# Kernel tuning notes

Hardware: AMD Instinct MI355X
Metric: run time of the kernel (lower is better)

Reference implementation:

```python
import jax, jax.numpy as jnp
import numpy as np

N = 10000
E = 320000
IN_DIM = 1
HD = 32
OUT_DIM = 1


def _lin(k, fan_in, fan_out):
    k1, k2 = jax.random.split(k)
    bound = 1.0 / np.sqrt(fan_in)
    W = jax.random.uniform(k1, (fan_in, fan_out), minval=-bound, maxval=bound, dtype=jnp.float32)
    b = jax.random.uniform(k2, (fan_out,), minval=-bound, maxval=bound, dtype=jnp.float32)
    return W, b


def setup_inputs() -> dict:
    key = jax.random.key(0)
    ks = jax.random.split(key, 12)
    sources = jax.random.randint(ks[0], (E,), 0, N)
    dests = jax.random.randint(ks[1], (E,), 0, N)
    weights = jax.random.uniform(ks[2], (E, 1), dtype=jnp.float32)
    x = jax.random.normal(ks[3], (N, IN_DIM), dtype=jnp.float32)
    h = jax.random.normal(ks[4], (N, HD), dtype=jnp.float32)
    W_enc, b_enc = _lin(ks[5], IN_DIM + HD, HD)
    W_msg, b_msg = _lin(ks[6], 2 * HD + 1, HD)
    W_upd, b_upd = _lin(ks[7], 2 * HD, HD)
    W_dec, b_dec = _lin(ks[8], 2 * HD, OUT_DIM)
    W_term, b_term = _lin(ks[9], HD, 1)
    W_pred, b_pred = _lin(ks[10], 2 * HD + 1, 1)
    return {"sources": sources, "dests": dests, "weights": weights, "x": x, "h": h,
            "W_enc": W_enc, "b_enc": b_enc, "W_msg": W_msg, "b_msg": b_msg,
            "W_upd": W_upd, "b_upd": b_upd, "W_dec": W_dec, "b_dec": b_dec,
            "W_term": W_term, "b_term": b_term, "W_pred": W_pred, "b_pred": b_pred}


def reference(sources, dests, weights, x, h, W_enc, b_enc, W_msg, b_msg,
              W_upd, b_upd, W_dec, b_dec, W_term, b_term, W_pred, b_pred):
    n = h.shape[0]
    # Encoder: z = Linear(cat[x, h])
    z = jnp.concatenate([x, h], axis=1) @ W_enc + b_enc  # [N, HD]
    # Processor messages: Linear(cat[z[dest], z[src], w])
    msg_in = jnp.concatenate([z[dests], z[sources], weights], axis=1)  # [E, 2*HD+1]
    messages = msg_in @ W_msg + b_msg  # [E, HD]
    # scatter-amax into destination nodes, -inf (no edge) -> 0
    m = jnp.full((n, HD), -jnp.inf, dtype=z.dtype).at[dests].max(messages)
    m = jnp.where(jnp.isneginf(m), jnp.zeros_like(m), m)
    h_new = jnp.concatenate([z, m], axis=1) @ W_upd + b_upd  # [N, HD]
    # Decoder
    y = jnp.concatenate([z, h_new], axis=1) @ W_dec + b_dec  # [N, 1]
    # Termination: proj of mean node state -> scalar
    t = (h_new.mean(axis=0) @ W_term + b_term).squeeze()
    # Predecessor: dense N x N score matrix, edge entries set to proj score
    pred_in = jnp.concatenate([h_new[dests], h_new[sources], weights], axis=1)
    edge_scores = (pred_in @ W_pred + b_pred)[:, 0]  # [E]
    p = jnp.full((n, n), -1e9, dtype=h_new.dtype).at[dests, sources].set(edge_scores)
    return (y, p, h_new, t)
```

## Files before the change

### kernel.cpp

```cpp
#include <hip/hip_runtime.h>
#include <stdint.h>

namespace {
constexpr int  kN  = 10000;
constexpr int  kE  = 320000;
constexpr long kPOff = 10000;
constexpr long kHOff = 10000L + 100000000L;
constexpr long kTOff = kHOff + 320000L;
}

typedef float f32x4 __attribute__((ext_vector_type(4)));

__device__ __forceinline__ float shfl32(float v, int k) { return __shfl(v, k, 32); }

__global__ __launch_bounds__(256) void encz_kernel(
    const float* __restrict__ x, const float* __restrict__ h,
    const float* __restrict__ W_enc, const float* __restrict__ b_enc,
    const float* __restrict__ W_msg, const float* __restrict__ b_msg,
    float* __restrict__ z, float* __restrict__ zwd, float* __restrict__ zws,
    float* __restrict__ m)
{
    int lane = threadIdx.x & 63;
    int wid  = threadIdx.x >> 6;
    int half = lane >> 5;
    int j    = lane & 31;
    int i = blockIdx.x * 8 + wid * 2 + half;
    if (i >= kN) return;

    float hj = h[(long)i * 32 + j];
    float xi = x[i];
    float zj = fmaf(xi, W_enc[j], b_enc[j]);
#pragma unroll
    for (int k = 0; k < 32; ++k)
        zj = fmaf(shfl32(hj, k), W_enc[(1 + k) * 32 + j], zj);

    z[(long)i * 32 + j] = zj;
    m[(long)i * 32 + j] = -__builtin_inff();

    float dv = b_msg[j], sv = 0.0f;
#pragma unroll
    for (int k = 0; k < 32; ++k) {
        float zk = shfl32(zj, k);
        dv = fmaf(zk, W_msg[k * 32 + j], dv);
        sv = fmaf(zk, W_msg[(32 + k) * 32 + j], sv);
    }
    zwd[(long)i * 32 + j] = dv;
    zws[(long)i * 32 + j] = sv;
}

__global__ __launch_bounds__(256) void msgmax_kernel(
    const int* __restrict__ src, const int* __restrict__ dst,
    const float* __restrict__ w, const float* __restrict__ zwd,
    const float* __restrict__ zws, const float* __restrict__ W_msg,
    float* __restrict__ m)
{
    int lane = threadIdx.x & 63;
    int wid  = threadIdx.x >> 6;
    int half = lane >> 5;
    int j    = lane & 31;
    float Ww = W_msg[64 * 32 + j];
    int gw = blockIdx.x * 4 + wid;
    int nw = gridDim.x * 4;
    for (int ep = gw; ep < kE / 2; ep += nw) {
        int e = ep * 2 + half;
        int d = dst[e], s = src[e];
        float val = fmaf(w[e], Ww, zwd[(long)d * 32 + j] + zws[(long)s * 32 + j]);
        float* addr = m + (long)d * 32 + j;
        if (val >= 0.0f)
            atomicMax(reinterpret_cast<int*>(addr), __float_as_int(val));
        else
            atomicMin(reinterpret_cast<unsigned int*>(addr), __float_as_uint(val));
    }
}

__global__ __launch_bounds__(256) void updn_kernel(
    const float* __restrict__ z, const float* __restrict__ m,
    const float* __restrict__ W_upd, const float* __restrict__ b_upd,
    const float* __restrict__ W_dec, const float* __restrict__ b_dec,
    const float* __restrict__ W_pred,
    float* __restrict__ y_out, float* __restrict__ h_out,
    float* __restrict__ a_out, float* __restrict__ b_out,
    float* __restrict__ partials)
{
    int i = blockIdx.x * 256 + threadIdx.x;
    bool valid = i < kN;
    int ii = valid ? i : (kN - 1);

    float acc[32];
#pragma unroll
    for (int jj = 0; jj < 32; ++jj) acc[jj] = b_upd[jj];
    float yv = b_dec[0];

    const float4* z4 = reinterpret_cast<const float4*>(z + (long)ii * 32);
#pragma unroll
    for (int q = 0; q < 8; ++q) {
        float4 v = z4[q];
        float in0 = v.x, in1 = v.y, in2 = v.z, in3 = v.w;
        int k = q * 4;
        yv = fmaf(in0, W_dec[k + 0], yv);
        yv = fmaf(in1, W_dec[k + 1], yv);
        yv = fmaf(in2, W_dec[k + 2], yv);
        yv = fmaf(in3, W_dec[k + 3], yv);
        const float* W0 = W_upd + (k + 0) * 32;
        const float* W1 = W_upd + (k + 1) * 32;
        const float* W2 = W_upd + (k + 2) * 32;
        const float* W3 = W_upd + (k + 3) * 32;
#pragma unroll
        for (int jj = 0; jj < 32; ++jj) acc[jj] = fmaf(in0, W0[jj], acc[jj]);
#pragma unroll
        for (int jj = 0; jj < 32; ++jj) acc[jj] = fmaf(in1, W1[jj], acc[jj]);
#pragma unroll
        for (int jj = 0; jj < 32; ++jj) acc[jj] = fmaf(in2, W2[jj], acc[jj]);
#pragma unroll
        for (int jj = 0; jj < 32; ++jj) acc[jj] = fmaf(in3, W3[jj], acc[jj]);
    }

    const float NEG_INF = -__builtin_inff();
    const float4* m4 = reinterpret_cast<const float4*>(m + (long)ii * 32);
#pragma unroll
    for (int q = 0; q < 8; ++q) {
        float4 v = m4[q];
        float in0 = (v.x == NEG_INF) ? 0.0f : v.x;
        float in1 = (v.y == NEG_INF) ? 0.0f : v.y;
        float in2 = (v.z == NEG_INF) ? 0.0f : v.z;
        float in3 = (v.w == NEG_INF) ? 0.0f : v.w;
        int k = 32 + q * 4;
        const float* W0 = W_upd + (k + 0) * 32;
        const float* W1 = W_upd + (k + 1) * 32;
        const float* W2 = W_upd + (k + 2) * 32;
        const float* W3 = W_upd + (k + 3) * 32;
#pragma unroll
        for (int jj = 0; jj < 32; ++jj) acc[jj] = fmaf(in0, W0[jj], acc[jj]);
#pragma unroll
        for (int jj = 0; jj < 32; ++jj) acc[jj] = fmaf(in1, W1[jj], acc[jj]);
#pragma unroll
        for (int jj = 0; jj < 32; ++jj) acc[jj] = fmaf(in2, W2[jj], acc[jj]);
#pragma unroll
        for (int jj = 0; jj < 32; ++jj) acc[jj] = fmaf(in3, W3[jj], acc[jj]);
    }

    float av = 0.0f, bv = 0.0f;
#pragma unroll
    for (int k = 0; k < 32; ++k) {
        yv = fmaf(acc[k], W_dec[32 + k], yv);
        av = fmaf(acc[k], W_pred[k], av);
        bv = fmaf(acc[k], W_pred[32 + k], bv);
    }

    if (valid) {
        y_out[i] = yv;
        a_out[i] = av;
        b_out[i] = bv;
        float4* hrow = reinterpret_cast<float4*>(h_out + (long)i * 32);
#pragma unroll
        for (int q = 0; q < 8; ++q)
            hrow[q] = make_float4(acc[q * 4 + 0], acc[q * 4 + 1], acc[q * 4 + 2], acc[q * 4 + 3]);
    }

    int wslot = blockIdx.x * 4 + ((threadIdx.x >> 6) & 3);
#pragma unroll
    for (int jj = 0; jj < 32; ++jj) {
        float v = valid ? acc[jj] : 0.0f;
#pragma unroll
        for (int off = 32; off; off >>= 1) v += __shfl_down(v, off, 64);
        if ((threadIdx.x & 63) == 0) partials[(long)wslot * 32 + jj] = v;
    }
}

__global__ void term_kernel(const float* __restrict__ partials,
                            const float* __restrict__ W_term,
                            const float* __restrict__ b_term,
                            float* __restrict__ t_out)
{
    int l = threadIdx.x;
    float s = 0.0f;
    if (l < 32) {
        for (int r = 0; r < 160; ++r) s += partials[(long)r * 32 + l];
        s = (s * (1.0f / (float)kN)) * W_term[l];
    }
#pragma unroll
    for (int off = 32; off; off >>= 1) s += __shfl_down(s, off, 64);
    if (l == 0) t_out[0] = s + b_term[0];
}

__global__ __launch_bounds__(256) void fill_kernel(float* __restrict__ p)
{
    long idx = (long)blockIdx.x * 256 + threadIdx.x;
    long stride = (long)gridDim.x * 256;
    const long total4 = (long)kN * (long)kN / 4;
    f32x4 v = { -1e9f, -1e9f, -1e9f, -1e9f };
    f32x4* p4 = reinterpret_cast<f32x4*>(p);
    for (long i = idx; i < total4; i += stride)
        p4[i] = v;
}

__global__ __launch_bounds__(256) void predl_kernel(
    const int* __restrict__ src, const int* __restrict__ dst,
    const float* __restrict__ w, const float* __restrict__ a,
    const float* __restrict__ b, const float* __restrict__ W_pred,
    const float* __restrict__ b_pred, float* __restrict__ p)
{
    int e = blockIdx.x * 256 + threadIdx.x;
    if (e >= kE) return;
    int d = dst[e], s = src[e];
    float score = a[d] + b[s] + fmaf(w[e], W_pred[64], b_pred[0]);
    p[(long)d * kN + s] = score;
}

extern "C" void kernel_launch(void* const* d_in, const int* in_sizes, int n_in,
                              void* d_out, int out_size, void* d_ws, size_t ws_size,
                              hipStream_t stream)
{
    const int*   sources = (const int*)d_in[0];
    const int*   dests   = (const int*)d_in[1];
    const float* weights = (const float*)d_in[2];
    const float* x       = (const float*)d_in[3];
    const float* h       = (const float*)d_in[4];
    const float* W_enc   = (const float*)d_in[5];
    const float* b_enc   = (const float*)d_in[6];
    const float* W_msg   = (const float*)d_in[7];
    const float* b_msg   = (const float*)d_in[8];
    const float* W_upd   = (const float*)d_in[9];
    const float* b_upd   = (const float*)d_in[10];
    const float* W_dec   = (const float*)d_in[11];
    const float* b_dec   = (const float*)d_in[12];
    const float* W_term  = (const float*)d_in[13];
    const float* b_term  = (const float*)d_in[14];
    const float* W_pred  = (const float*)d_in[15];
    const float* b_pred  = (const float*)d_in[16];

    float* out   = (float*)d_out;
    float* y_out = out;
    float* p_out = out + kPOff;
    float* h_out = out + kHOff;
    float* t_out = out + kTOff;

    float* z        = (float*)d_ws;
    float* m        = z   + (long)kN * 32;
    float* zwd      = m   + (long)kN * 32;
    float* zws      = zwd + (long)kN * 32;
    float* a_ws     = zws + (long)kN * 32;
    float* b_ws     = a_ws + kN;
    float* partials = b_ws + kN;

    encz_kernel<<<(kN + 7) / 8, 256, 0, stream>>>(x, h, W_enc, b_enc, W_msg, b_msg,
                                                  z, zwd, zws, m);
    msgmax_kernel<<<10000, 256, 0, stream>>>(sources, dests, weights, zwd, zws, W_msg, m);
    updn_kernel<<<(kN + 255) / 256, 256, 0, stream>>>(z, m, W_upd, b_upd, W_dec, b_dec,
                                                      W_pred, y_out, h_out, a_ws, b_ws,
                                                      partials);
    term_kernel<<<1, 64, 0, stream>>>(partials, W_term, b_term, t_out);
    fill_kernel<<<8192, 256, 0, stream>>>(p_out);
    predl_kernel<<<(kE + 255) / 256, 256, 0, stream>>>(sources, dests, weights, a_ws, b_ws,
                                                       W_pred, b_pred, p_out);
}
```

Baseline: 557.4 us.

## Replace atomic scatter-max with CSR build and per-node gather-max

Builds a destination-sorted edge list (degree histogram, single-block scan, atomic scatter into an edge list stored temporarily in the p output buffer), then computes each node's max message with a per-node gather loop instead of per-element float atomics. This removes atomic contention on the m buffer and the -inf init/fixup, and writes m directly with the zero fallback. It adds four extra kernel launches, a serial single-block scan, and a data-dependent loop whose length follows node degree. It also relies on fill_kernel later overwriting the reused p buffer.

After: 586.7 us. 5.3% more time.

```diff
diff --git a/kernel.cpp b/kernel.cpp
--- a/kernel.cpp
+++ b/kernel.cpp
@@ -18,8 +18,11 @@
     const float* __restrict__ W_enc, const float* __restrict__ b_enc,
     const float* __restrict__ W_msg, const float* __restrict__ b_msg,
     float* __restrict__ z, float* __restrict__ zwd, float* __restrict__ zws,
-    float* __restrict__ m)
-{
+    int* __restrict__ deg, int* __restrict__ cursor)
+{
+    int t = blockIdx.x * 256 + threadIdx.x;
+    if (t < kN) { deg[t] = 0; cursor[t] = 0; }
+
     int lane = threadIdx.x & 63;
     int wid  = threadIdx.x >> 6;
     int half = lane >> 5;
@@ -35,7 +38,6 @@
         zj = fmaf(shfl32(hj, k), W_enc[(1 + k) * 32 + j], zj);
 
     z[(long)i * 32 + j] = zj;
-    m[(long)i * 32 + j] = -__builtin_inff();
 
     float dv = b_msg[j], sv = 0.0f;
 #pragma unroll
@@ -48,29 +50,90 @@
     zws[(long)i * 32 + j] = sv;
 }
 
-__global__ __launch_bounds__(256) void msgmax_kernel(
-    const int* __restrict__ src, const int* __restrict__ dst,
-    const float* __restrict__ w, const float* __restrict__ zwd,
-    const float* __restrict__ zws, const float* __restrict__ W_msg,
+__global__ __launch_bounds__(256) void hist_kernel(const int* __restrict__ dst,
+                                                   int* __restrict__ deg)
+{
+    int e = blockIdx.x * 256 + threadIdx.x;
+    if (e < kE) atomicAdd(&deg[dst[e]], 1);
+}
+
+__global__ __launch_bounds__(256) void scan_kernel(const int* __restrict__ deg,
+                                                   int* __restrict__ rowptr)
+{
+    __shared__ int part[256];
+    const int CH = 40;
+    int t = threadIdx.x;
+    int vals[CH];
+    int local = 0;
+#pragma unroll
+    for (int i = 0; i < CH; ++i) {
+        int idx = t * CH + i;
+        int v = (idx < kN) ? deg[idx] : 0;
+        vals[i] = local;
+        local += v;
+    }
+    part[t] = local;
+    __syncthreads();
+    for (int off = 1; off < 256; off <<= 1) {
+        int v = (t >= off) ? part[t - off] : 0;
+        __syncthreads();
+        part[t] += v;
+        __syncthreads();
+    }
+    int excl = part[t] - local;
+#pragma unroll
+    for (int i = 0; i < CH; ++i) {
+        int idx = t * CH + i;
+        if (idx < kN) rowptr[idx] = excl + vals[i];
+    }
+}
+
+__global__ __launch_bounds__(256) void scatter_kernel(
+    const int* __restrict__ dst, const int* __restrict__ rowptr,
+    int* __restrict__ cursor, int* __restrict__ elist)
+{
+    int e = blockIdx.x * 256 + threadIdx.x;
+    if (e >= kE) return;
+    int d = dst[e];
+    int pos = atomicAdd(&cursor[d], 1);
+    elist[rowptr[d] + pos] = e;
+}
+
+__global__ __launch_bounds__(256) void gathermax_kernel(
+    const int* __restrict__ src, const float* __restrict__ w,
+    const float* __restrict__ zwd, const float* __restrict__ zws,
+    const int* __restrict__ rowptr, const int* __restrict__ deg,
+    const int* __restrict__ elist, const float* __restrict__ W_msg,
     float* __restrict__ m)
 {
     int lane = threadIdx.x & 63;
     int wid  = threadIdx.x >> 6;
     int half = lane >> 5;
     int j    = lane & 31;
+    int d = blockIdx.x * 8 + wid * 2 + half;
+    if (d >= kN) return;
+
     float Ww = W_msg[64 * 32 + j];
-    int gw = blockIdx.x * 4 + wid;
-    int nw = gridDim.x * 4;
-    for (int ep = gw; ep < kE / 2; ep += nw) {
-        int e = ep * 2 + half;
-        int d = dst[e], s = src[e];
-        float val = fmaf(w[e], Ww, zwd[(long)d * 32 + j] + zws[(long)s * 32 + j]);
-        float* addr = m + (long)d * 32 + j;
-        if (val >= 0.0f)
-            atomicMax(reinterpret_cast<int*>(addr), __float_as_int(val));
-        else
-            atomicMin(reinterpret_cast<unsigned int*>(addr), __float_as_uint(val));
-    }
+    float partial = zwd[(long)d * 32 + j];
+    float mx = -__builtin_inff();
+    int base = rowptr[d], cnt = deg[d];
+
+    if (cnt > 0) {
+        int e = elist[base];
+        int s = src[e];
+        float we = w[e];
+        for (int i = 1; i < cnt; ++i) {
+            int e2 = elist[base + i];
+            int s2 = src[e2];
+            float we2 = w[e2];
+            float msg = fmaf(we, Ww, partial + zws[(long)s * 32 + j]);
+            mx = fmaxf(mx, msg);
+            s = s2; we = we2;
+        }
+        float msg = fmaf(we, Ww, partial + zws[(long)s * 32 + j]);
+        mx = fmaxf(mx, msg);
+    }
+    m[(long)d * 32 + j] = (mx == -__builtin_inff()) ? 0.0f : mx;
 }
 
 __global__ __launch_bounds__(256) void updn_kernel(
@@ -242,10 +305,18 @@
     float* a_ws     = zws + (long)kN * 32;
     float* b_ws     = a_ws + kN;
     float* partials = b_ws + kN;
+    int*   deg      = (int*)(partials + 160 * 32);
+    int*   rowptr   = deg + kN;
+    int*   cursor   = rowptr + kN;
+    int*   elist    = (int*)p_out;
 
     encz_kernel<<<(kN + 7) / 8, 256, 0, stream>>>(x, h, W_enc, b_enc, W_msg, b_msg,
-                                                  z, zwd, zws, m);
-    msgmax_kernel<<<10000, 256, 0, stream>>>(sources, dests, weights, zwd, zws, W_msg, m);
+                                                  z, zwd, zws, deg, cursor);
+    hist_kernel<<<(kE + 255) / 256, 256, 0, stream>>>(dests, deg);
+    scan_kernel<<<1, 256, 0, stream>>>(deg, rowptr);
+    scatter_kernel<<<(kE + 255) / 256, 256, 0, stream>>>(dests, rowptr, cursor, elist);
+    gathermax_kernel<<<(kN + 7) / 8, 256, 0, stream>>>(sources, weights, zwd, zws,
+                                                       rowptr, deg, elist, W_msg, m);
     updn_kernel<<<(kN + 255) / 256, 256, 0, stream>>>(z, m, W_upd, b_upd, W_dec, b_dec,
                                                       W_pred, y_out, h_out, a_ws, b_ws,
                                                       partials);
```

## Spread dense score-matrix fill across compute kernels and merge termination into pred

Applied to the files above, without the earlier changes.

The 400MB fill of the -1e9 score matrix is split into three slices, each appended to the encoder, message-max and update kernels, so the bandwidth-bound fill runs alongside the latency-bound gather and atomic work. All kernels use a fixed grid of 2048 blocks with grid-stride loops. The separate term kernel is removed by accumulating the node-state sum with atomicAdd and computing t inside the pred kernel. This adds atomic float additions, which make the summation order nondeterministic, and fixes the fill split ratios by hand.

After: 599.1 us. 1.07x slower.

```diff
diff --git a/kernel.cpp b/kernel.cpp
--- a/kernel.cpp
+++ b/kernel.cpp
@@ -7,52 +7,70 @@
 constexpr long kPOff = 10000;
 constexpr long kHOff = 10000L + 100000000L;
 constexpr long kTOff = kHOff + 320000L;
+constexpr long kP4   = (long)kN * kN / 4;
+constexpr long kFillA = kP4 * 15 / 100;
+constexpr long kFillB = kP4 * 80 / 100;
+constexpr int  kG = 2048;
 }
 
 typedef float f32x4 __attribute__((ext_vector_type(4)));
 
 __device__ __forceinline__ float shfl32(float v, int k) { return __shfl(v, k, 32); }
 
-__global__ __launch_bounds__(256) void encz_kernel(
+__device__ __forceinline__ void fill_slice(float* __restrict__ p, long lo, long hi)
+{
+    long idx = (long)blockIdx.x * blockDim.x + threadIdx.x;
+    long stride = (long)gridDim.x * blockDim.x;
+    f32x4 v = { -1e9f, -1e9f, -1e9f, -1e9f };
+    f32x4* p4 = reinterpret_cast<f32x4*>(p);
+    for (long i = lo + idx; i < hi; i += stride)
+        p4[i] = v;
+}
+
+__global__ __launch_bounds__(256) void k1_encz(
     const float* __restrict__ x, const float* __restrict__ h,
     const float* __restrict__ W_enc, const float* __restrict__ b_enc,
     const float* __restrict__ W_msg, const float* __restrict__ b_msg,
     float* __restrict__ z, float* __restrict__ zwd, float* __restrict__ zws,
-    float* __restrict__ m)
-{
+    float* __restrict__ m, float* __restrict__ sum_h, float* __restrict__ p)
+{
+    if (blockIdx.x == 0 && threadIdx.x < 32) sum_h[threadIdx.x] = 0.0f;
+
     int lane = threadIdx.x & 63;
     int wid  = threadIdx.x >> 6;
     int half = lane >> 5;
     int j    = lane & 31;
-    int i = blockIdx.x * 8 + wid * 2 + half;
-    if (i >= kN) return;
-
-    float hj = h[(long)i * 32 + j];
-    float xi = x[i];
-    float zj = fmaf(xi, W_enc[j], b_enc[j]);
-#pragma unroll
-    for (int k = 0; k < 32; ++k)
-        zj = fmaf(shfl32(hj, k), W_enc[(1 + k) * 32 + j], zj);
-
-    z[(long)i * 32 + j] = zj;
-    m[(long)i * 32 + j] = -__builtin_inff();
-
-    float dv = b_msg[j], sv = 0.0f;
-#pragma unroll
-    for (int k = 0; k < 32; ++k) {
-        float zk = shfl32(zj, k);
-        dv = fmaf(zk, W_msg[k * 32 + j], dv);
-        sv = fmaf(zk, W_msg[(32 + k) * 32 + j], sv);
-    }
-    zwd[(long)i * 32 + j] = dv;
-    zws[(long)i * 32 + j] = sv;
-}
-
-__global__ __launch_bounds__(256) void msgmax_kernel(
+
+    for (int i = blockIdx.x * 8 + wid * 2 + half; i < kN; i += kG * 8) {
+        float hj = h[(long)i * 32 + j];
+        float xi = x[i];
+        float zj = fmaf(xi, W_enc[j], b_enc[j]);
+#pragma unroll
+        for (int k = 0; k < 32; ++k)
+            zj = fmaf(shfl32(hj, k), W_enc[(1 + k) * 32 + j], zj);
+
+        z[(long)i * 32 + j] = zj;
+        m[(long)i * 32 + j] = -__builtin_inff();
+
+        float dv = b_msg[j], sv = 0.0f;
+#pragma unroll
+        for (int k = 0; k < 32; ++k) {
+            float zk = shfl32(zj, k);
+            dv = fmaf(zk, W_msg[k * 32 + j], dv);
+            sv = fmaf(zk, W_msg[(32 + k) * 32 + j], sv);
+        }
+        zwd[(long)i * 32 + j] = dv;
+        zws[(long)i * 32 + j] = sv;
+    }
+
+    fill_slice(p, 0, kFillA);
+}
+
+__global__ __launch_bounds__(256) void k2_msgmax(
     const int* __restrict__ src, const int* __restrict__ dst,
     const float* __restrict__ w, const float* __restrict__ zwd,
     const float* __restrict__ zws, const float* __restrict__ W_msg,
-    float* __restrict__ m)
+    float* __restrict__ m, float* __restrict__ p)
 {
     int lane = threadIdx.x & 63;
     int wid  = threadIdx.x >> 6;
@@ -60,8 +78,7 @@
     int j    = lane & 31;
     float Ww = W_msg[64 * 32 + j];
     int gw = blockIdx.x * 4 + wid;
-    int nw = gridDim.x * 4;
-    for (int ep = gw; ep < kE / 2; ep += nw) {
+    for (int ep = gw; ep < kE / 2; ep += kG * 4) {
         int e = ep * 2 + half;
         int d = dst[e], s = src[e];
         float val = fmaf(w[e], Ww, zwd[(long)d * 32 + j] + zws[(long)s * 32 + j]);
@@ -71,140 +88,129 @@
         else
             atomicMin(reinterpret_cast<unsigned int*>(addr), __float_as_uint(val));
     }
-}
-
-__global__ __launch_bounds__(256) void updn_kernel(
+
+    fill_slice(p, kFillA, kFillB);
+}
+
+__global__ __launch_bounds__(256) void k3_updn(
     const float* __restrict__ z, const float* __restrict__ m,
     const float* __restrict__ W_upd, const float* __restrict__ b_upd,
     const float* __restrict__ W_dec, const float* __restrict__ b_dec,
     const float* __restrict__ W_pred,
     float* __restrict__ y_out, float* __restrict__ h_out,
     float* __restrict__ a_out, float* __restrict__ b_out,
-    float* __restrict__ partials)
+    float* __restrict__ sum_h, float* __restrict__ p)
 {
     int i = blockIdx.x * 256 + threadIdx.x;
-    bool valid = i < kN;
-    int ii = valid ? i : (kN - 1);
-
-    float acc[32];
-#pragma unroll
-    for (int jj = 0; jj < 32; ++jj) acc[jj] = b_upd[jj];
-    float yv = b_dec[0];
-
-    const float4* z4 = reinterpret_cast<const float4*>(z + (long)ii * 32);
-#pragma unroll
-    for (int q = 0; q < 8; ++q) {
-        float4 v = z4[q];
-        float in0 = v.x, in1 = v.y, in2 = v.z, in3 = v.w;
-        int k = q * 4;
-        yv = fmaf(in0, W_dec[k + 0], yv);
-        yv = fmaf(in1, W_dec[k + 1], yv);
-        yv = fmaf(in2, W_dec[k + 2], yv);
-        yv = fmaf(in3, W_dec[k + 3], yv);
-        const float* W0 = W_upd + (k + 0) * 32;
-        const float* W1 = W_upd + (k + 1) * 32;
-        const float* W2 = W_upd + (k + 2) * 32;
-        const float* W3 = W_upd + (k + 3) * 32;
-#pragma unroll
-        for (int jj = 0; jj < 32; ++jj) acc[jj] = fmaf(in0, W0[jj], acc[jj]);
-#pragma unroll
-        for (int jj = 0; jj < 32; ++jj) acc[jj] = fmaf(in1, W1[jj], acc[jj]);
-#pragma unroll
-        for (int jj = 0; jj < 32; ++jj) acc[jj] = fmaf(in2, W2[jj], acc[jj]);
-#pragma unroll
-        for (int jj = 0; jj < 32; ++jj) acc[jj] = fmaf(in3, W3[jj], acc[jj]);
-    }
-
-    const float NEG_INF = -__builtin_inff();
-    const float4* m4 = reinterpret_cast<const float4*>(m + (long)ii * 32);
-#pragma unroll
-    for (int q = 0; q < 8; ++q) {
-        float4 v = m4[q];
-        float in0 = (v.x == NEG_INF) ? 0.0f : v.x;
-        float in1 = (v.y == NEG_INF) ? 0.0f : v.y;
-        float in2 = (v.z == NEG_INF) ? 0.0f : v.z;
-        float in3 = (v.w == NEG_INF) ? 0.0f : v.w;
-        int k = 32 + q * 4;
-        const float* W0 = W_upd + (k + 0) * 32;
-        const float* W1 = W_upd + (k + 1) * 32;
-        const float* W2 = W_upd + (k + 2) * 32;
-        const float* W3 = W_upd + (k + 3) * 32;
-#pragma unroll
-        for (int jj = 0; jj < 32; ++jj) acc[jj] = fmaf(in0, W0[jj], acc[jj]);
-#pragma unroll
-        for (int jj = 0; jj < 32; ++jj) acc[jj] = fmaf(in1, W1[jj], acc[jj]);
-#pragma unroll
-        for (int jj = 0; jj < 32; ++jj) acc[jj] = fmaf(in2, W2[jj], acc[jj]);
-#pragma unroll
-        for (int jj = 0; jj < 32; ++jj) acc[jj] = fmaf(in3, W3[jj], acc[jj]);
-    }
-
-    float av = 0.0f, bv = 0.0f;
-#pragma unroll
-    for (int k = 0; k < 32; ++k) {
-        yv = fmaf(acc[k], W_dec[32 + k], yv);
-        av = fmaf(acc[k], W_pred[k], av);
-        bv = fmaf(acc[k], W_pred[32 + k], bv);
-    }
-
-    if (valid) {
-        y_out[i] = yv;
-        a_out[i] = av;
-        b_out[i] = bv;
-        float4* hrow = reinterpret_cast<float4*>(h_out + (long)i * 32);
-#pragma unroll
-        for (int q = 0; q < 8; ++q)
-            hrow[q] = make_float4(acc[q * 4 + 0], acc[q * 4 + 1], acc[q * 4 + 2], acc[q * 4 + 3]);
-    }
-
-    int wslot = blockIdx.x * 4 + ((threadIdx.x >> 6) & 3);
-#pragma unroll
-    for (int jj = 0; jj < 32; ++jj) {
-        float v = valid ? acc[jj] : 0.0f;
-#pragma unroll
-        for (int off = 32; off; off >>= 1) v += __shfl_down(v, off, 64);
-        if ((threadIdx.x & 63) == 0) partials[(long)wslot * 32 + jj] = v;
-    }
-}
-
-__global__ void term_kernel(const float* __restrict__ partials,
-                            const float* __restrict__ W_term,
-                            const float* __restrict__ b_term,
-                            float* __restrict__ t_out)
-{
-    int l = threadIdx.x;
-    float s = 0.0f;
-    if (l < 32) {
-        for (int r = 0; r < 160; ++r) s += partials[(long)r * 32 + l];
-        s = (s * (1.0f / (float)kN)) * W_term[l];
-    }
-#pragma unroll
-    for (int off = 32; off; off >>= 1) s += __shfl_down(s, off, 64);
-    if (l == 0) t_out[0] = s + b_term[0];
-}
-
-__global__ __launch_bounds__(256) void fill_kernel(float* __restrict__ p)
-{
-    long idx = (long)blockIdx.x * 256 + threadIdx.x;
-    long stride = (long)gridDim.x * 256;
-    const long total4 = (long)kN * (long)kN / 4;
-    f32x4 v = { -1e9f, -1e9f, -1e9f, -1e9f };
-    f32x4* p4 = reinterpret_cast<f32x4*>(p);
-    for (long i = idx; i < total4; i += stride)
-        p4[i] = v;
-}
-
-__global__ __launch_bounds__(256) void predl_kernel(
+    if (i < ((kN + 255) & ~255)) {
+        bool valid = i < kN;
+        int ii = valid ? i : (kN - 1);
+
+        float acc[32];
+#pragma unroll
+        for (int jj = 0; jj < 32; ++jj) acc[jj] = b_upd[jj];
+        float yv = b_dec[0];
+
+        const float4* z4 = reinterpret_cast<const float4*>(z + (long)ii * 32);
+#pragma unroll
+        for (int q = 0; q < 8; ++q) {
+            float4 v = z4[q];
+            float in0 = v.x, in1 = v.y, in2 = v.z, in3 = v.w;
+            int k = q * 4;
+            yv = fmaf(in0, W_dec[k + 0], yv);
+            yv = fmaf(in1, W_dec[k + 1], yv);
+            yv = fmaf(in2, W_dec[k + 2], yv);
+            yv = fmaf(in3, W_dec[k + 3], yv);
+            const float* W0 = W_upd + (k + 0) * 32;
+            const float* W1 = W_upd + (k + 1) * 32;
+            const float* W2 = W_upd + (k + 2) * 32;
+            const float* W3 = W_upd + (k + 3) * 32;
+#pragma unroll
+            for (int jj = 0; jj < 32; ++jj) acc[jj] = fmaf(in0, W0[jj], acc[jj]);
+#pragma unroll
+            for (int jj = 0; jj < 32; ++jj) acc[jj] = fmaf(in1, W1[jj], acc[jj]);
+#pragma unroll
+            for (int jj = 0; jj < 32; ++jj) acc[jj] = fmaf(in2, W2[jj], acc[jj]);
+#pragma unroll
+            for (int jj = 0; jj < 32; ++jj) acc[jj] = fmaf(in3, W3[jj], acc[jj]);
+        }
+
+        const float NEG_INF = -__builtin_inff();
+        const float4* m4 = reinterpret_cast<const float4*>(m + (long)ii * 32);
+#pragma unroll
+        for (int q = 0; q < 8; ++q) {
+            float4 v = m4[q];
+            float in0 = (v.x == NEG_INF) ? 0.0f : v.x;
+            float in1 = (v.y == NEG_INF) ? 0.0f : v.y;
+            float in2 = (v.z == NEG_INF) ? 0.0f : v.z;
+            float in3 = (v.w == NEG_INF) ? 0.0f : v.w;
+            int k = 32 + q * 4;
+            const float* W0 = W_upd + (k + 0) * 32;
+            const float* W1 = W_upd + (k + 1) * 32;
+            const float* W2 = W_upd + (k + 2) * 32;
+            const float* W3 = W_upd + (k + 3) * 32;
+#pragma unroll
+            for (int jj = 0; jj < 32; ++jj) acc[jj] = fmaf(in0, W0[jj], acc[jj]);
+#pragma unroll
+            for (int jj = 0; jj < 32; ++jj) acc[jj] = fmaf(in1, W1[jj], acc[jj]);
+#pragma unroll
+            for (int jj = 0; jj < 32; ++jj) acc[jj] = fmaf(in2, W2[jj], acc[jj]);
+#pragma unroll
+            for (int jj = 0; jj < 32; ++jj) acc[jj] = fmaf(in3, W3[jj], acc[jj]);
+        }
+
+        float av = 0.0f, bv = 0.0f;
+#pragma unroll
+        for (int k = 0; k < 32; ++k) {
+            yv = fmaf(acc[k], W_dec[32 + k], yv);
+            av = fmaf(acc[k], W_pred[k], av);
+            bv = fmaf(acc[k], W_pred[32 + k], bv);
+        }
+
+        if (valid) {
+            y_out[i] = yv;
+            a_out[i] = av;
+            b_out[i] = bv;
+            float4* hrow = reinterpret_cast<float4*>(h_out + (long)i * 32);
+#pragma unroll
+            for (int q = 0; q < 8; ++q)
+                hrow[q] = make_float4(acc[q * 4 + 0], acc[q * 4 + 1],
+                                      acc[q * 4 + 2], acc[q * 4 + 3]);
+        }
+
+#pragma unroll
+        for (int jj = 0; jj < 32; ++jj) {
+            float v = valid ? acc[jj] : 0.0f;
+#pragma unroll
+            for (int off = 32; off; off >>= 1) v += __shfl_down(v, off, 64);
+            if ((threadIdx.x & 63) == 0) atomicAdd(sum_h + jj, v);
+        }
+    }
+
+    fill_slice(p, kFillB, kP4);
+}
+
+__global__ __launch_bounds__(256) void k4_pred(
     const int* __restrict__ src, const int* __restrict__ dst,
     const float* __restrict__ w, const float* __restrict__ a,
     const float* __restrict__ b, const float* __restrict__ W_pred,
-    const float* __restrict__ b_pred, float* __restrict__ p)
-{
-    int e = blockIdx.x * 256 + threadIdx.x;
-    if (e >= kE) return;
-    int d = dst[e], s = src[e];
-    float score = a[d] + b[s] + fmaf(w[e], W_pred[64], b_pred[0]);
-    p[(long)d * kN + s] = score;
+    const float* __restrict__ b_pred, const float* __restrict__ sum_h,
+    const float* __restrict__ W_term, const float* __restrict__ b_term,
+    float* __restrict__ t_out, float* __restrict__ p)
+{
+    if (blockIdx.x == 0 && threadIdx.x < 64) {
+        int l = threadIdx.x;
+        float s = (l < 32) ? (sum_h[l] * (1.0f / (float)kN)) * W_term[l] : 0.0f;
+#pragma unroll
+        for (int off = 32; off; off >>= 1) s += __shfl_down(s, off, 64);
+        if (l == 0) t_out[0] = s + b_term[0];
+    }
+
+    for (int e = blockIdx.x * 256 + threadIdx.x; e < kE; e += kG * 256) {
+        int d = dst[e], s = src[e];
+        float score = a[d] + b[s] + fmaf(w[e], W_pred[64], b_pred[0]);
+        p[(long)d * kN + s] = score;
+    }
 }
 
 extern "C" void kernel_launch(void* const* d_in, const int* in_sizes, int n_in,
@@ -235,22 +241,21 @@
     float* h_out = out + kHOff;
     float* t_out = out + kTOff;
 
-    float* z        = (float*)d_ws;
-    float* m        = z   + (long)kN * 32;
-    float* zwd      = m   + (long)kN * 32;
-    float* zws      = zwd + (long)kN * 32;
-    float* a_ws     = zws + (long)kN * 32;
-    float* b_ws     = a_ws + kN;
-    float* partials = b_ws + kN;
-
-    encz_kernel<<<(kN + 7) / 8, 256, 0, stream>>>(x, h, W_enc, b_enc, W_msg, b_msg,
-                                                  z, zwd, zws, m);
-    msgmax_kernel<<<10000, 256, 0, stream>>>(sources, dests, weights, zwd, zws, W_msg, m);
-    updn_kernel<<<(kN + 255) / 256, 256, 0, stream>>>(z, m, W_upd, b_upd, W_dec, b_dec,
-                                                      W_pred, y_out, h_out, a_ws, b_ws,
-                                                      partials);
-    term_kernel<<<1, 64, 0, stream>>>(partials, W_term, b_term, t_out);
-    fill_kernel<<<8192, 256, 0, stream>>>(p_out);
-    predl_kernel<<<(kE + 255) / 256, 256, 0, stream>>>(sources, dests, weights, a_ws, b_ws,
-                                                       W_pred, b_pred, p_out);
-}
+    float* z     = (float*)d_ws;
+    float* m     = z   + (long)kN * 32;
+    float* zwd   = m   + (long)kN * 32;
+    float* zws   = zwd + (long)kN * 32;
+    float* a_ws  = zws + (long)kN * 32;
+    float* b_ws  = a_ws + kN;
+    float* sum_h = b_ws + kN;
+
+    k1_encz<<<kG, 256, 0, stream>>>(x, h, W_enc, b_enc, W_msg, b_msg,
+                                    z, zwd, zws, m, sum_h, p_out);
+    k2_msgmax<<<kG, 256, 0, stream>>>(sources, dests, weights, zwd, zws, W_msg,
+                                      m, p_out);
+    k3_updn<<<kG, 256, 0, stream>>>(z, m, W_upd, b_upd, W_dec, b_dec, W_pred,
+                                    y_out, h_out, a_ws, b_ws, sum_h, p_out);
+    k4_pred<<<kG, 256, 0, stream>>>(sources, dests, weights, a_ws, b_ws,
+                                    W_pred, b_pred, sum_h, W_term, b_term,
+                                    t_out, p_out);
+}
```

## Merge dense fill into encoder launch and fold termination into pred kernel

Applied to the files above, without the earlier changes.

The 400MB fill of the dense score matrix now runs as extra blocks of the encoder kernel, so the fill proceeds alongside the encoder instead of in its own launch after the update stage. The termination reduction is moved into block 0 of the predecessor-scatter kernel, dropping a tiny single-block launch. This cuts the launch count from six to four. The fill grid is halved to 4096 blocks, and the fill now runs before the message atomics, which could change how much of the 400MB write stays in cache.

Measured after the change: 560.6 us. About the same (+0.6%).

```diff
diff --git a/kernel.cpp b/kernel.cpp
--- a/kernel.cpp
+++ b/kernel.cpp
@@ -7,19 +7,33 @@
 constexpr long kPOff = 10000;
 constexpr long kHOff = 10000L + 100000000L;
 constexpr long kTOff = kHOff + 320000L;
+constexpr long kP4   = (long)kN * kN / 4;
+constexpr int  kEncBlocks  = (kN + 7) / 8;
+constexpr int  kFillBlocks = 4096;
 }
 
 typedef float f32x4 __attribute__((ext_vector_type(4)));
 
 __device__ __forceinline__ float shfl32(float v, int k) { return __shfl(v, k, 32); }
 
-__global__ __launch_bounds__(256) void encz_kernel(
+__global__ __launch_bounds__(256) void k1_encz_fill(
     const float* __restrict__ x, const float* __restrict__ h,
     const float* __restrict__ W_enc, const float* __restrict__ b_enc,
     const float* __restrict__ W_msg, const float* __restrict__ b_msg,
     float* __restrict__ z, float* __restrict__ zwd, float* __restrict__ zws,
-    float* __restrict__ m)
-{
+    float* __restrict__ m, float* __restrict__ p)
+{
+    if (blockIdx.x >= kEncBlocks) {
+        long fb = blockIdx.x - kEncBlocks;
+        long idx = fb * 256 + threadIdx.x;
+        long stride = (long)kFillBlocks * 256;
+        f32x4 v = { -1e9f, -1e9f, -1e9f, -1e9f };
+        f32x4* p4 = reinterpret_cast<f32x4*>(p);
+        for (long i = idx; i < kP4; i += stride)
+            p4[i] = v;
+        return;
+    }
+
     int lane = threadIdx.x & 63;
     int wid  = threadIdx.x >> 6;
     int half = lane >> 5;
@@ -48,7 +62,7 @@
     zws[(long)i * 32 + j] = sv;
 }
 
-__global__ __launch_bounds__(256) void msgmax_kernel(
+__global__ __launch_bounds__(256) void k2_msgmax(
     const int* __restrict__ src, const int* __restrict__ dst,
     const float* __restrict__ w, const float* __restrict__ zwd,
     const float* __restrict__ zws, const float* __restrict__ W_msg,
@@ -73,7 +87,7 @@
     }
 }
 
-__global__ __launch_bounds__(256) void updn_kernel(
+__global__ __launch_bounds__(256) void k3_updn(
     const float* __restrict__ z, const float* __restrict__ m,
     const float* __restrict__ W_upd, const float* __restrict__ b_upd,
     const float* __restrict__ W_dec, const float* __restrict__ b_dec,
@@ -154,7 +168,8 @@
         float4* hrow = reinterpret_cast<float4*>(h_out + (long)i * 32);
 #pragma unroll
         for (int q = 0; q < 8; ++q)
-            hrow[q] = make_float4(acc[q * 4 + 0], acc[q * 4 + 1], acc[q * 4 + 2], acc[q * 4 + 3]);
+            hrow[q] = make_float4(acc[q * 4 + 0], acc[q * 4 + 1],
+                                  acc[q * 4 + 2], acc[q * 4 + 3]);
     }
 
     int wslot = blockIdx.x * 4 + ((threadIdx.x >> 6) & 3);
@@ -167,39 +182,26 @@
     }
 }
 
-__global__ void term_kernel(const float* __restrict__ partials,
-                            const float* __restrict__ W_term,
-                            const float* __restrict__ b_term,
-                            float* __restrict__ t_out)
-{
-    int l = threadIdx.x;
-    float s = 0.0f;
-    if (l < 32) {
-        for (int r = 0; r < 160; ++r) s += partials[(long)r * 32 + l];
-        s = (s * (1.0f / (float)kN)) * W_term[l];
-    }
-#pragma unroll
-    for (int off = 32; off; off >>= 1) s += __shfl_down(s, off, 64);
-    if (l == 0) t_out[0] = s + b_term[0];
-}
-
-__global__ __launch_bounds__(256) void fill_kernel(float* __restrict__ p)
-{
-    long idx = (long)blockIdx.x * 256 + threadIdx.x;
-    long stride = (long)gridDim.x * 256;
-    const long total4 = (long)kN * (long)kN / 4;
-    f32x4 v = { -1e9f, -1e9f, -1e9f, -1e9f };
-    f32x4* p4 = reinterpret_cast<f32x4*>(p);
-    for (long i = idx; i < total4; i += stride)
-        p4[i] = v;
-}
-
-__global__ __launch_bounds__(256) void predl_kernel(
+__global__ __launch_bounds__(256) void k4_pred(
     const int* __restrict__ src, const int* __restrict__ dst,
     const float* __restrict__ w, const float* __restrict__ a,
     const float* __restrict__ b, const float* __restrict__ W_pred,
-    const float* __restrict__ b_pred, float* __restrict__ p)
-{
+    const float* __restrict__ b_pred, const float* __restrict__ partials,
+    const float* __restrict__ W_term, const float* __restrict__ b_term,
+    float* __restrict__ t_out, float* __restrict__ p)
+{
+    if (blockIdx.x == 0 && threadIdx.x < 64) {
+        int l = threadIdx.x;
+        float s = 0.0f;
+        if (l < 32) {
+            for (int r = 0; r < 160; ++r) s += partials[(long)r * 32 + l];
+            s = (s * (1.0f / (float)kN)) * W_term[l];
+        }
+#pragma unroll
+        for (int off = 32; off; off >>= 1) s += __shfl_down(s, off, 64);
+        if (l == 0) t_out[0] = s + b_term[0];
+    }
+
     int e = blockIdx.x * 256 + threadIdx.x;
     if (e >= kE) return;
     int d = dst[e], s = src[e];
@@ -243,14 +245,13 @@
     float* b_ws     = a_ws + kN;
     float* partials = b_ws + kN;
 
-    encz_kernel<<<(kN + 7) / 8, 256, 0, stream>>>(x, h, W_enc, b_enc, W_msg, b_msg,
-                                                  z, zwd, zws, m);
-    msgmax_kernel<<<10000, 256, 0, stream>>>(sources, dests, weights, zwd, zws, W_msg, m);
-    updn_kernel<<<(kN + 255) / 256, 256, 0, stream>>>(z, m, W_upd, b_upd, W_dec, b_dec,
-                                                      W_pred, y_out, h_out, a_ws, b_ws,
-                                                      partials);
-    term_kernel<<<1, 64, 0, stream>>>(partials, W_term, b_term, t_out);
-    fill_kernel<<<8192, 256, 0, stream>>>(p_out);
-    predl_kernel<<<(kE + 255) / 256, 256, 0, stream>>>(sources, dests, weights, a_ws, b_ws,
-                                                       W_pred, b_pred, p_out);
-}
+    k1_encz_fill<<<kEncBlocks + kFillBlocks, 256, 0, stream>>>(
+        x, h, W_enc, b_enc, W_msg, b_msg, z, zwd, zws, m, p_out);
+    k2_msgmax<<<10000, 256, 0, stream>>>(sources, dests, weights, zwd, zws, W_msg, m);
+    k3_updn<<<(kN + 255) / 256, 256, 0, stream>>>(z, m, W_upd, b_upd, W_dec, b_dec,
+                                                  W_pred, y_out, h_out, a_ws, b_ws,
+                                                  partials);
+    k4_pred<<<(kE + 255) / 256, 256, 0, stream>>>(sources, dests, weights, a_ws, b_ws,
+                                                  W_pred, b_pred, partials, W_term, b_term,
+                                                  t_out, p_out);
+}
```
